# Performance work log

Hardware: AMD Instinct MI355X
Metric: run time of the kernel (lower is better)

## Reference

```python
import jax, jax.numpy as jnp
import numpy as np

BN_EPS = 1e-5
N_NODES = 100000
N_EDGES = 1600000
F_IN = 128
F_HID = 256
N_ITEMS = 128


def setup_inputs() -> dict:
    key = jax.random.key(0)
    ks = jax.random.split(key, 6)
    return {
        "node_feature": jax.random.normal(ks[0], (N_NODES, F_IN), jnp.float32),
        "edge_index": jax.random.randint(ks[1], (2, N_EDGES), 0, N_NODES, jnp.int64),
        "items_ready_to_cache": jnp.arange(N_ITEMS, dtype=jnp.int64),
        "gcn_w": jax.random.normal(ks[2], (F_IN, F_HID), jnp.float32) / np.sqrt(F_IN),
        "gcn_b": jnp.zeros((F_HID,), jnp.float32),
        "bn_gamma": jnp.ones((F_HID,), jnp.float32),
        "bn_beta": jnp.zeros((F_HID,), jnp.float32),
        "emb_table": jax.random.normal(ks[3], (F_IN, F_IN), jnp.float32),
        "proj_w": jax.random.normal(ks[4], (F_HID, F_IN), jnp.float32) / np.sqrt(F_HID),
        "proj_b": jnp.zeros((F_IN,), jnp.float32),
    }


def _gcn_conv(x, edge_index, w, b, n_nodes):
    # PyG GCNConv: add self-loops, symmetric normalization, scatter-add to target.
    loop = jnp.arange(n_nodes, dtype=edge_index.dtype)
    src = jnp.concatenate([edge_index[0], loop])
    dst = jnp.concatenate([edge_index[1], loop])
    h = x @ w                                  # [N, F_HID]
    deg = jax.ops.segment_sum(jnp.ones_like(dst, dtype=h.dtype), dst,
                              num_segments=n_nodes)
    dinv = jnp.where(deg > 0, jax.lax.rsqrt(deg), 0.0)
    norm = dinv[src] * dinv[dst]               # [E+N]
    msgs = h[src] * norm[:, None]              # gather + scale  [E+N, F_HID]
    out = jax.ops.segment_sum(msgs, dst, num_segments=n_nodes)  # scatter-add
    return out + b


def reference(node_feature, edge_index, items_ready_to_cache, gcn_w, gcn_b,
              bn_gamma, bn_beta, emb_table, proj_w, proj_b):
    n_nodes = node_feature.shape[0]
    x = _gcn_conv(node_feature, edge_index, gcn_w, gcn_b, n_nodes)
    # BatchNorm1d in training mode: batch stats (biased variance)
    mean = jnp.mean(x, axis=0)
    var = jnp.mean((x - mean) ** 2, axis=0)
    x = bn_gamma * (x - mean) * jax.lax.rsqrt(var + BN_EPS) + bn_beta
    x = jax.nn.relu(x)
    rsu_embedding = x[0:1] @ proj_w + proj_b   # [1, F_IN]
    # item_id_to_index collapses indices to arange(len(items))
    n_items = items_ready_to_cache.shape[0]
    items_embeddings = emb_table[jnp.arange(n_items)]  # [n_items, F_IN]
    scores = items_embeddings @ rsu_embedding[0]       # [n_items]
    return scores, rsu_embedding
```

## Files before the change

### kernel.cpp

```cpp
#include <hip/hip_runtime.h>
#include <hip/hip_bf16.h>


#define THREADS 256

__global__ __launch_bounds__(THREADS) void deg_kernel(const int* __restrict__ ei,
                                                      int* __restrict__ deg, int E, int N) {
    int e = blockIdx.x * THREADS + threadIdx.x;
    if (e < E) {
        unsigned d = (unsigned)ei[E + e];
        if (d < (unsigned)N) atomicAdd(&deg[d], 1);
    }
}

__global__ __launch_bounds__(THREADS) void dinv_kernel(const int* __restrict__ deg,
                                                       float* __restrict__ dinv, int n) {
    int i = blockIdx.x * THREADS + threadIdx.x;
    if (i < n) dinv[i] = rsqrtf((float)(deg[i] + 1));
}

__global__ __launch_bounds__(THREADS) void scan1_kernel(const int* __restrict__ deg,
                                                        int* __restrict__ rowptr,
                                                        int* __restrict__ bsum, int n) {
    __shared__ int sh[THREADS];
    const int t = threadIdx.x, b = blockIdx.x;
    const int base = b * 1024 + t * 4;
    int v0 = (base + 0 < n) ? deg[base + 0] : 0;
    int v1 = (base + 1 < n) ? deg[base + 1] : 0;
    int v2 = (base + 2 < n) ? deg[base + 2] : 0;
    int v3 = (base + 3 < n) ? deg[base + 3] : 0;
    const int local = v0 + v1 + v2 + v3;
    sh[t] = local;
    __syncthreads();
    int run = local;
    for (int off = 1; off < THREADS; off <<= 1) {
        int add = (t >= off) ? sh[t - off] : 0;
        __syncthreads();
        run += add;
        sh[t] = run;
        __syncthreads();
    }
    const int excl = run - local;
    if (base + 0 < n) rowptr[base + 0] = excl;
    if (base + 1 < n) rowptr[base + 1] = excl + v0;
    if (base + 2 < n) rowptr[base + 2] = excl + v0 + v1;
    if (base + 3 < n) rowptr[base + 3] = excl + v0 + v1 + v2;
    if (t == 0) bsum[b] = sh[THREADS - 1];
}

__global__ __launch_bounds__(THREADS) void scan2_kernel(const int* __restrict__ bsum,
                                                        int* __restrict__ boff, int nb) {
    __shared__ int sh[THREADS];
    const int t = threadIdx.x;
    const int local = (t < nb) ? bsum[t] : 0;
    sh[t] = local;
    __syncthreads();
    int run = local;
    for (int off = 1; off < THREADS; off <<= 1) {
        int add = (t >= off) ? sh[t - off] : 0;
        __syncthreads();
        run += add;
        sh[t] = run;
        __syncthreads();
    }
    boff[t] = run - local;
}

__global__ __launch_bounds__(THREADS) void scan3_kernel(int* __restrict__ rowptr,
                                                        int* __restrict__ cursor,
                                                        const int* __restrict__ boff,
                                                        int n, int E) {
    int i = blockIdx.x * THREADS + threadIdx.x;
    if (i < n) {
        int v = rowptr[i] + boff[i >> 10];
        rowptr[i] = v;
        cursor[i] = v;
    }
    if (i == 0) rowptr[n] = E;
}

__global__ __launch_bounds__(THREADS) void scatter_kernel(const int* __restrict__ ei,
                                                          int* __restrict__ cursor,
                                                          int* __restrict__ csr,
                                                          int E, int N) {
    int e = blockIdx.x * THREADS + threadIdx.x;
    if (e < E) {
        unsigned d = (unsigned)ei[E + e];
        if (d < (unsigned)N) {
            int p = atomicAdd(&cursor[d], 1);
            if ((unsigned)p < (unsigned)E) csr[p] = ei[e];
        }
    }
}

__device__ __forceinline__ float2 agg_row(const float* __restrict__ x,
                                          const int* __restrict__ rowptr,
                                          const int* __restrict__ csr,
                                          const float* __restrict__ dinv,
                                          int i, int n, int lane) {
    const int e0 = rowptr[i], e1 = rowptr[i + 1];
    const float di = dinv[i];
    const float2 xs = *(const float2*)(x + (size_t)i * 128 + lane * 2);
    float ax = di * xs.x, ay = di * xs.y;
    int e = e0;
    for (; e + 4 <= e1; e += 4) {
        int s0 = csr[e],     s1 = csr[e + 1], s2 = csr[e + 2], s3 = csr[e + 3];
        s0 = ((unsigned)s0 < (unsigned)n) ? s0 : 0;
        s1 = ((unsigned)s1 < (unsigned)n) ? s1 : 0;
        s2 = ((unsigned)s2 < (unsigned)n) ? s2 : 0;
        s3 = ((unsigned)s3 < (unsigned)n) ? s3 : 0;
        float w0 = dinv[s0], w1 = dinv[s1], w2 = dinv[s2], w3 = dinv[s3];
        float2 p0 = *(const float2*)(x + (size_t)s0 * 128 + lane * 2);
        float2 p1 = *(const float2*)(x + (size_t)s1 * 128 + lane * 2);
        float2 p2 = *(const float2*)(x + (size_t)s2 * 128 + lane * 2);
        float2 p3 = *(const float2*)(x + (size_t)s3 * 128 + lane * 2);
        ax = fmaf(w0, p0.x, ax); ay = fmaf(w0, p0.y, ay);
        ax = fmaf(w1, p1.x, ax); ay = fmaf(w1, p1.y, ay);
        ax = fmaf(w2, p2.x, ax); ay = fmaf(w2, p2.y, ay);
        ax = fmaf(w3, p3.x, ax); ay = fmaf(w3, p3.y, ay);
    }
    for (; e < e1; ++e) {
        int s = csr[e];
        s = ((unsigned)s < (unsigned)n) ? s : 0;
        float w = dinv[s];
        float2 p = *(const float2*)(x + (size_t)s * 128 + lane * 2);
        ax = fmaf(w, p.x, ax); ay = fmaf(w, p.y, ay);
    }
    return make_float2(di * ax, di * ay);
}

__global__ __launch_bounds__(THREADS) void agg_kernel(const float* __restrict__ x,
                                                      const int* __restrict__ rowptr,
                                                      const int* __restrict__ csr,
                                                      const float* __restrict__ dinv,
                                                      float* __restrict__ agg, int n) {
    const int lane = threadIdx.x & 63;
    const int wid  = blockIdx.x * (THREADS >> 6) + (threadIdx.x >> 6);
    const int nw   = gridDim.x * (THREADS >> 6);
    for (int i = wid; i < n; i += nw) {
        float2 o = agg_row(x, rowptr, csr, dinv, i, n, lane);
        *(float2*)(agg + (size_t)i * 128 + lane * 2) = o;
    }
}

__device__ __forceinline__ void gemm_epilogue(float acc[4][16], float* red,
                                              const float* __restrict__ bias,
                                              float* __restrict__ colsum,
                                              float* __restrict__ colsumsq,
                                              float* __restrict__ row0,
                                              int rowbase, int n, int tx, int ty, int t,
                                              int blockIdx_x) {
    bool valid[4];
#pragma unroll
    for (int i = 0; i < 4; ++i) valid[i] = (rowbase + ty * 4 + i) < n;
#pragma unroll
    for (int j = 0; j < 16; ++j) {
        float bj = bias[tx * 16 + j];
#pragma unroll
        for (int i = 0; i < 4; ++i)
            if (valid[i]) acc[i][j] += bj;
    }
    if (blockIdx_x == 0 && ty == 0) {
#pragma unroll
        for (int j = 0; j < 16; ++j) row0[tx * 16 + j] = acc[0][j];
    }
    float s[16], q[16];
#pragma unroll
    for (int j = 0; j < 16; ++j) {
        s[j] = 0.f; q[j] = 0.f;
#pragma unroll
        for (int i = 0; i < 4; ++i) {
            s[j] += acc[i][j];
            q[j] = fmaf(acc[i][j], acc[i][j], q[j]);
        }
    }
    float* redS = red;
    float* redQ = red + 16 * 256;
#pragma unroll
    for (int j = 0; j < 16; ++j) {
        redS[ty * 256 + tx * 16 + j] = s[j];
        redQ[ty * 256 + tx * 16 + j] = q[j];
    }
    __syncthreads();
    float S = 0.f, Q = 0.f;
#pragma unroll
    for (int g = 0; g < 16; ++g) {
        S += redS[g * 256 + t];
        Q += redQ[g * 256 + t];
    }
    atomicAdd(&colsum[t], S);
    atomicAdd(&colsumsq[t], Q);
}

__global__ __launch_bounds__(THREADS) void gemm_stats_kernel(
        const float* __restrict__ A, const float* __restrict__ W,
        const float* __restrict__ bias, float* __restrict__ colsum,
        float* __restrict__ colsumsq, float* __restrict__ row0, int n) {
    __shared__ float Asm[64 * 36];
    __shared__ float Bsm[32 * 320];
    const int t = threadIdx.x;
    const int tx = t & 15, ty = t >> 4;
    const int rowbase = blockIdx.x * 64;

    float acc[4][16];
#pragma unroll
    for (int i = 0; i < 4; ++i)
#pragma unroll
        for (int j = 0; j < 16; ++j) acc[i][j] = 0.0f;

    for (int kk = 0; kk < 128; kk += 32) {
#pragma unroll
        for (int u = 0; u < 2; ++u) {
            int f4 = t * 2 + u;
            int r = f4 >> 3, c4 = f4 & 7;
            int gr = rowbase + r;
            float4 v = make_float4(0.f, 0.f, 0.f, 0.f);
            if (gr < n) v = *(const float4*)(A + (size_t)gr * 128 + kk + c4 * 4);
            *(float4*)(Asm + r * 36 + c4 * 4) = v;
        }
#pragma unroll
        for (int u = 0; u < 8; ++u) {
            int f4 = t + u * 256;
            int k = f4 >> 6, c4 = f4 & 63;
            float4 v = *(const float4*)(W + (size_t)(kk + k) * 256 + c4 * 4);
            int blk = c4 >> 2, l = (c4 & 3) * 4;
            *(float4*)(Bsm + k * 320 + blk * 20 + l) = v;
        }
        __syncthreads();
#pragma unroll 4
        for (int k = 0; k < 32; ++k) {
            float a[4];
#pragma unroll
            for (int i = 0; i < 4; ++i) a[i] = Asm[(ty * 4 + i) * 36 + k];
            const float* bp = Bsm + k * 320 + tx * 20;
            float4 b0 = *(const float4*)(bp);
            float4 b1 = *(const float4*)(bp + 4);
            float4 b2 = *(const float4*)(bp + 8);
            float4 b3 = *(const float4*)(bp + 12);
            float bb[16] = {b0.x, b0.y, b0.z, b0.w, b1.x, b1.y, b1.z, b1.w,
                            b2.x, b2.y, b2.z, b2.w, b3.x, b3.y, b3.z, b3.w};
#pragma unroll
            for (int i = 0; i < 4; ++i)
#pragma unroll
                for (int j = 0; j < 16; ++j) acc[i][j] = fmaf(a[i], bb[j], acc[i][j]);
        }
        __syncthreads();
    }
    gemm_epilogue(acc, Bsm, bias, colsum, colsumsq, row0, rowbase, n, tx, ty, t,
                  blockIdx.x);
}

__global__ __launch_bounds__(THREADS) void fused_agg_gemm_kernel(
        const float* __restrict__ x, const int* __restrict__ rowptr,
        const int* __restrict__ csr, const float* __restrict__ dinv,
        const float* __restrict__ W, const float* __restrict__ bias,
        float* __restrict__ colsum, float* __restrict__ colsumsq,
        float* __restrict__ row0, int n) {
    __shared__ float Asm[64 * 132];
    __shared__ float Bsm[16 * 320];
    const int t = threadIdx.x;
    const int lane = t & 63, wv = t >> 6;
    const int tx = t & 15, ty = t >> 4;
    const int rowbase = blockIdx.x * 64;

    for (int rr = 0; rr < 16; ++rr) {
        const int r = wv * 16 + rr;
        const int i = rowbase + r;
        float2 o = make_float2(0.f, 0.f);
        if (i < n) o = agg_row(x, rowptr, csr, dinv, i, n, lane);
        *(float2*)(Asm + r * 132 + lane * 2) = o;
    }
    __syncthreads();

    float acc[4][16];
#pragma unroll
    for (int i = 0; i < 4; ++i)
#pragma unroll
        for (int j = 0; j < 16; ++j) acc[i][j] = 0.0f;

    for (int kk = 0; kk < 128; kk += 16) {
#pragma unroll
        for (int u = 0; u < 4; ++u) {
            int f4 = t + u * 256;
            int k = f4 >> 6, c4 = f4 & 63;
            float4 v = *(const float4*)(W + (size_t)(kk + k) * 256 + c4 * 4);
            int blk = c4 >> 2, l = (c4 & 3) * 4;
            *(float4*)(Bsm + k * 320 + blk * 20 + l) = v;
        }
        __syncthreads();
#pragma unroll 4
        for (int k = 0; k < 16; ++k) {
            float a[4];
#pragma unroll
            for (int i = 0; i < 4; ++i) a[i] = Asm[(ty * 4 + i) * 132 + kk + k];
            const float* bp = Bsm + k * 320 + tx * 20;
            float4 b0 = *(const float4*)(bp);
            float4 b1 = *(const float4*)(bp + 4);
            float4 b2 = *(const float4*)(bp + 8);
            float4 b3 = *(const float4*)(bp + 12);
            float bb[16] = {b0.x, b0.y, b0.z, b0.w, b1.x, b1.y, b1.z, b1.w,
                            b2.x, b2.y, b2.z, b2.w, b3.x, b3.y, b3.z, b3.w};
#pragma unroll
            for (int i = 0; i < 4; ++i)
#pragma unroll
                for (int j = 0; j < 16; ++j) acc[i][j] = fmaf(a[i], bb[j], acc[i][j]);
        }
        __syncthreads();
    }
    gemm_epilogue(acc, Asm, bias, colsum, colsumsq, row0, rowbase, n, tx, ty, t,
                  blockIdx.x);
}

__global__ __launch_bounds__(THREADS) void finalize_kernel(
        const float* __restrict__ colsum, const float* __restrict__ colsumsq,
        const float* __restrict__ row0, const float* __restrict__ gamma,
        const float* __restrict__ beta, const float* __restrict__ proj_w,
        const float* __restrict__ proj_b, const float* __restrict__ emb,
        float* __restrict__ out, int n_nodes, int n_items) {
    __shared__ float x0[256];
    __shared__ float rsu[128];
    const int t = threadIdx.x;
    const float invn = 1.0f / (float)n_nodes;
    {
        float mean = colsum[t] * invn;
        float var = colsumsq[t] * invn - mean * mean;
        float r = rsqrtf(var + 1e-5f);
        float v = gamma[t] * (row0[t] - mean) * r + beta[t];
        x0[t] = v > 0.f ? v : 0.f;
    }
    __syncthreads();
    if (t < 128) {
        float sacc = proj_b[t];
        for (int c = 0; c < 256; ++c) sacc = fmaf(x0[c], proj_w[c * 128 + t], sacc);
        rsu[t] = sacc;
        out[128 + t] = sacc;
    }
    __syncthreads();
    if (t < n_items) {
        float sacc = 0.f;
        for (int j = 0; j < 128; ++j) sacc = fmaf(emb[t * 128 + j], rsu[j], sacc);
        out[t] = sacc;
    }
}

extern "C" void kernel_launch(void* const* d_in, const int* in_sizes, int n_in,
                              void* d_out, int out_size, void* d_ws, size_t ws_size,
                              hipStream_t stream) {
    const float* node_feature = (const float*)d_in[0];
    const int*   edge_index   = (const int*)d_in[1];
    const float* gcn_w  = (const float*)d_in[3];
    const float* gcn_b  = (const float*)d_in[4];
    const float* bn_g   = (const float*)d_in[5];
    const float* bn_b   = (const float*)d_in[6];
    const float* emb    = (const float*)d_in[7];
    const float* proj_w = (const float*)d_in[8];
    const float* proj_b = (const float*)d_in[9];
    float* out = (float*)d_out;

    const int N = in_sizes[0] / 128;
    const int E = in_sizes[1] / 2;
    const int n_items = in_sizes[2];

    char* base = (char*)d_ws;
    size_t off = 0;
    auto alloc = [&](size_t bytes) -> void* {
        void* p = (void*)(base + off);
        off += (bytes + 255) & ~(size_t)255;
        return p;
    };
    int*   deg      = (int*)alloc((size_t)N * 4);
    float* dinv     = (float*)alloc((size_t)N * 4);
    int*   rowptr   = (int*)alloc(((size_t)N + 1) * 4);
    int*   cursor   = (int*)alloc((size_t)N * 4);
    int*   bsum     = (int*)alloc(256 * 4);
    int*   boff     = (int*)alloc(256 * 4);
    float* colsum   = (float*)alloc(256 * 4);
    float* colsumsq = (float*)alloc(256 * 4);
    float* row0     = (float*)alloc(256 * 4);
    int*   csr      = (int*)alloc((size_t)E * 4);
    const size_t fused_need = off;
    float* agg      = (float*)alloc((size_t)N * 128 * 4);
    const size_t split_need = off;
    const bool use_split = (ws_size >= split_need);
    (void)fused_need;

    const int nbE = (E + THREADS - 1) / THREADS;
    const int nbN = (N + THREADS - 1) / THREADS;
    const int nchunks = (N + 1023) >> 10;
    const int nbRow = (N + 63) / 64;

    hipMemsetAsync(deg, 0, (size_t)N * 4, stream);
    hipMemsetAsync(colsum, 0, 2 * 256 * 4, stream);

    deg_kernel<<<nbE, THREADS, 0, stream>>>(edge_index, deg, E, N);
    dinv_kernel<<<nbN, THREADS, 0, stream>>>(deg, dinv, N);
    scan1_kernel<<<nchunks, THREADS, 0, stream>>>(deg, rowptr, bsum, N);
    scan2_kernel<<<1, THREADS, 0, stream>>>(bsum, boff, nchunks);
    scan3_kernel<<<nbN, THREADS, 0, stream>>>(rowptr, cursor, boff, N, E);
    scatter_kernel<<<nbE, THREADS, 0, stream>>>(edge_index, cursor, csr, E, N);
    if (use_split) {
        agg_kernel<<<2048, THREADS, 0, stream>>>(node_feature, rowptr, csr, dinv,
                                                 agg, N);
        gemm_stats_kernel<<<nbRow, THREADS, 0, stream>>>(agg, gcn_w, gcn_b,
                                                         colsum, colsumsq, row0, N);
    } else {
        fused_agg_gemm_kernel<<<nbRow, THREADS, 0, stream>>>(node_feature, rowptr,
                                                             csr, dinv, gcn_w, gcn_b,
                                                             colsum, colsumsq, row0, N);
    }
    finalize_kernel<<<1, THREADS, 0, stream>>>(colsum, colsumsq, row0, bn_g, bn_b,
                                               proj_w, proj_b, emb, out, N, n_items);
}
```

Baseline: 522.1 us.

## Replace per-node GEMM with Gram-matrix statistics and rank-based CSR build

Instead of computing the full N x 256 GCN output, the aggregated features (128-wide) are reduced to a 128x128 Gram matrix and a column sum. BatchNorm mean and variance are then derived algebraically via W^T G W, with the bias term added analytically, and row 0 is computed separately. The CSR build records each edge's atomic rank during the degree pass, which removes the cursor atomics and the scan3 pass, and it folds dinv into scan1. The aggregation uses a persistent work-stealing kernel with per-block partial Grams that are reduced afterwards. The trade-off is some precision risk from the E[x^2]-mean^2 form and large partial-Gram workspace traffic.

```diff
diff --git a/kernel.cpp b/kernel.cpp
--- a/kernel.cpp
+++ b/kernel.cpp
@@ -4,24 +4,23 @@
 
 #define THREADS 256
 
-__global__ __launch_bounds__(THREADS) void deg_kernel(const int* __restrict__ ei,
-                                                      int* __restrict__ deg, int E, int N) {
+__global__ __launch_bounds__(THREADS) void deg_rank_kernel(const int* __restrict__ ei,
+                                                           int* __restrict__ deg,
+                                                           int* __restrict__ rank,
+                                                           int E, int N) {
     int e = blockIdx.x * THREADS + threadIdx.x;
     if (e < E) {
         unsigned d = (unsigned)ei[E + e];
-        if (d < (unsigned)N) atomicAdd(&deg[d], 1);
-    }
-}
-
-__global__ __launch_bounds__(THREADS) void dinv_kernel(const int* __restrict__ deg,
-                                                       float* __restrict__ dinv, int n) {
-    int i = blockIdx.x * THREADS + threadIdx.x;
-    if (i < n) dinv[i] = rsqrtf((float)(deg[i] + 1));
+        int p = 0;
+        if (d < (unsigned)N) p = atomicAdd(&deg[d], 1);
+        rank[e] = p;
+    }
 }
 
 __global__ __launch_bounds__(THREADS) void scan1_kernel(const int* __restrict__ deg,
                                                         int* __restrict__ rowptr,
-                                                        int* __restrict__ bsum, int n) {
+                                                        int* __restrict__ bsum,
+                                                        float* __restrict__ dinv, int n) {
     __shared__ int sh[THREADS];
     const int t = threadIdx.x, b = blockIdx.x;
     const int base = b * 1024 + t * 4;
@@ -29,6 +28,10 @@
     int v1 = (base + 1 < n) ? deg[base + 1] : 0;
     int v2 = (base + 2 < n) ? deg[base + 2] : 0;
     int v3 = (base + 3 < n) ? deg[base + 3] : 0;
+    if (base + 0 < n) dinv[base + 0] = rsqrtf((float)(v0 + 1));
+    if (base + 1 < n) dinv[base + 1] = rsqrtf((float)(v1 + 1));
+    if (base + 2 < n) dinv[base + 2] = rsqrtf((float)(v2 + 1));
+    if (base + 3 < n) dinv[base + 3] = rsqrtf((float)(v3 + 1));
     const int local = v0 + v1 + v2 + v3;
     sh[t] = local;
     __syncthreads();
@@ -49,7 +52,10 @@
 }
 
 __global__ __launch_bounds__(THREADS) void scan2_kernel(const int* __restrict__ bsum,
-                                                        int* __restrict__ boff, int nb) {
+                                                        int* __restrict__ boff, int nb,
+                                                        float* __restrict__ colsumS,
+                                                        float* __restrict__ G,
+                                                        int* __restrict__ workctr) {
     __shared__ int sh[THREADS];
     const int t = threadIdx.x;
     const int local = (t < nb) ? bsum[t] : 0;
@@ -64,251 +70,177 @@
         __syncthreads();
     }
     boff[t] = run - local;
-}
-
-__global__ __launch_bounds__(THREADS) void scan3_kernel(int* __restrict__ rowptr,
-                                                        int* __restrict__ cursor,
-                                                        const int* __restrict__ boff,
-                                                        int n, int E) {
-    int i = blockIdx.x * THREADS + threadIdx.x;
-    if (i < n) {
-        int v = rowptr[i] + boff[i >> 10];
-        rowptr[i] = v;
-        cursor[i] = v;
-    }
-    if (i == 0) rowptr[n] = E;
+    if (t < 128) colsumS[t] = 0.f;
+    if (t == 0) *workctr = 0;
+    for (int u = t; u < 16384; u += THREADS) G[u] = 0.f;
 }
 
 __global__ __launch_bounds__(THREADS) void scatter_kernel(const int* __restrict__ ei,
-                                                          int* __restrict__ cursor,
+                                                          const int* __restrict__ rowptr,
+                                                          const int* __restrict__ boff,
+                                                          const int* __restrict__ rank,
                                                           int* __restrict__ csr,
                                                           int E, int N) {
     int e = blockIdx.x * THREADS + threadIdx.x;
     if (e < E) {
         unsigned d = (unsigned)ei[E + e];
         if (d < (unsigned)N) {
-            int p = atomicAdd(&cursor[d], 1);
-            if ((unsigned)p < (unsigned)E) csr[p] = ei[e];
+            int base = rowptr[d] + boff[d >> 10] + rank[e];
+            if ((unsigned)base < (unsigned)E) csr[base] = ei[e];
         }
     }
 }
 
-__device__ __forceinline__ float2 agg_row(const float* __restrict__ x,
-                                          const int* __restrict__ rowptr,
-                                          const int* __restrict__ csr,
-                                          const float* __restrict__ dinv,
-                                          int i, int n, int lane) {
-    const int e0 = rowptr[i], e1 = rowptr[i + 1];
-    const float di = dinv[i];
-    const float2 xs = *(const float2*)(x + (size_t)i * 128 + lane * 2);
-    float ax = di * xs.x, ay = di * xs.y;
-    int e = e0;
-    for (; e + 4 <= e1; e += 4) {
-        int s0 = csr[e],     s1 = csr[e + 1], s2 = csr[e + 2], s3 = csr[e + 3];
-        s0 = ((unsigned)s0 < (unsigned)n) ? s0 : 0;
-        s1 = ((unsigned)s1 < (unsigned)n) ? s1 : 0;
-        s2 = ((unsigned)s2 < (unsigned)n) ? s2 : 0;
-        s3 = ((unsigned)s3 < (unsigned)n) ? s3 : 0;
-        float w0 = dinv[s0], w1 = dinv[s1], w2 = dinv[s2], w3 = dinv[s3];
-        float2 p0 = *(const float2*)(x + (size_t)s0 * 128 + lane * 2);
-        float2 p1 = *(const float2*)(x + (size_t)s1 * 128 + lane * 2);
-        float2 p2 = *(const float2*)(x + (size_t)s2 * 128 + lane * 2);
-        float2 p3 = *(const float2*)(x + (size_t)s3 * 128 + lane * 2);
-        ax = fmaf(w0, p0.x, ax); ay = fmaf(w0, p0.y, ay);
-        ax = fmaf(w1, p1.x, ax); ay = fmaf(w1, p1.y, ay);
-        ax = fmaf(w2, p2.x, ax); ay = fmaf(w2, p2.y, ay);
-        ax = fmaf(w3, p3.x, ax); ay = fmaf(w3, p3.y, ay);
-    }
-    for (; e < e1; ++e) {
-        int s = csr[e];
-        s = ((unsigned)s < (unsigned)n) ? s : 0;
-        float w = dinv[s];
-        float2 p = *(const float2*)(x + (size_t)s * 128 + lane * 2);
-        ax = fmaf(w, p.x, ax); ay = fmaf(w, p.y, ay);
-    }
-    return make_float2(di * ax, di * ay);
-}
-
-__global__ __launch_bounds__(THREADS) void agg_kernel(const float* __restrict__ x,
-                                                      const int* __restrict__ rowptr,
-                                                      const int* __restrict__ csr,
-                                                      const float* __restrict__ dinv,
-                                                      float* __restrict__ agg, int n) {
-    const int lane = threadIdx.x & 63;
-    const int wid  = blockIdx.x * (THREADS >> 6) + (threadIdx.x >> 6);
-    const int nw   = gridDim.x * (THREADS >> 6);
-    for (int i = wid; i < n; i += nw) {
-        float2 o = agg_row(x, rowptr, csr, dinv, i, n, lane);
-        *(float2*)(agg + (size_t)i * 128 + lane * 2) = o;
-    }
-}
-
-__device__ __forceinline__ void gemm_epilogue(float acc[4][16], float* red,
-                                              const float* __restrict__ bias,
-                                              float* __restrict__ colsum,
-                                              float* __restrict__ colsumsq,
-                                              float* __restrict__ row0,
-                                              int rowbase, int n, int tx, int ty, int t,
-                                              int blockIdx_x) {
-    bool valid[4];
-#pragma unroll
-    for (int i = 0; i < 4; ++i) valid[i] = (rowbase + ty * 4 + i) < n;
-#pragma unroll
-    for (int j = 0; j < 16; ++j) {
-        float bj = bias[tx * 16 + j];
-#pragma unroll
-        for (int i = 0; i < 4; ++i)
-            if (valid[i]) acc[i][j] += bj;
-    }
-    if (blockIdx_x == 0 && ty == 0) {
-#pragma unroll
-        for (int j = 0; j < 16; ++j) row0[tx * 16 + j] = acc[0][j];
-    }
-    float s[16], q[16];
-#pragma unroll
-    for (int j = 0; j < 16; ++j) {
-        s[j] = 0.f; q[j] = 0.f;
-#pragma unroll
-        for (int i = 0; i < 4; ++i) {
-            s[j] += acc[i][j];
-            q[j] = fmaf(acc[i][j], acc[i][j], q[j]);
-        }
-    }
-    float* redS = red;
-    float* redQ = red + 16 * 256;
-#pragma unroll
-    for (int j = 0; j < 16; ++j) {
-        redS[ty * 256 + tx * 16 + j] = s[j];
-        redQ[ty * 256 + tx * 16 + j] = q[j];
-    }
-    __syncthreads();
-    float S = 0.f, Q = 0.f;
-#pragma unroll
-    for (int g = 0; g < 16; ++g) {
-        S += redS[g * 256 + t];
-        Q += redQ[g * 256 + t];
-    }
-    atomicAdd(&colsum[t], S);
-    atomicAdd(&colsumsq[t], Q);
-}
-
-__global__ __launch_bounds__(THREADS) void gemm_stats_kernel(
-        const float* __restrict__ A, const float* __restrict__ W,
-        const float* __restrict__ bias, float* __restrict__ colsum,
-        float* __restrict__ colsumsq, float* __restrict__ row0, int n) {
-    __shared__ float Asm[64 * 36];
-    __shared__ float Bsm[32 * 320];
-    const int t = threadIdx.x;
-    const int tx = t & 15, ty = t >> 4;
-    const int rowbase = blockIdx.x * 64;
-
-    float acc[4][16];
-#pragma unroll
-    for (int i = 0; i < 4; ++i)
-#pragma unroll
-        for (int j = 0; j < 16; ++j) acc[i][j] = 0.0f;
-
-    for (int kk = 0; kk < 128; kk += 32) {
-#pragma unroll
-        for (int u = 0; u < 2; ++u) {
-            int f4 = t * 2 + u;
-            int r = f4 >> 3, c4 = f4 & 7;
-            int gr = rowbase + r;
-            float4 v = make_float4(0.f, 0.f, 0.f, 0.f);
-            if (gr < n) v = *(const float4*)(A + (size_t)gr * 128 + kk + c4 * 4);
-            *(float4*)(Asm + r * 36 + c4 * 4) = v;
-        }
-#pragma unroll
-        for (int u = 0; u < 8; ++u) {
-            int f4 = t + u * 256;
-            int k = f4 >> 6, c4 = f4 & 63;
-            float4 v = *(const float4*)(W + (size_t)(kk + k) * 256 + c4 * 4);
-            int blk = c4 >> 2, l = (c4 & 3) * 4;
-            *(float4*)(Bsm + k * 320 + blk * 20 + l) = v;
-        }
-        __syncthreads();
-#pragma unroll 4
-        for (int k = 0; k < 32; ++k) {
-            float a[4];
-#pragma unroll
-            for (int i = 0; i < 4; ++i) a[i] = Asm[(ty * 4 + i) * 36 + k];
-            const float* bp = Bsm + k * 320 + tx * 20;
-            float4 b0 = *(const float4*)(bp);
-            float4 b1 = *(const float4*)(bp + 4);
-            float4 b2 = *(const float4*)(bp + 8);
-            float4 b3 = *(const float4*)(bp + 12);
-            float bb[16] = {b0.x, b0.y, b0.z, b0.w, b1.x, b1.y, b1.z, b1.w,
-                            b2.x, b2.y, b2.z, b2.w, b3.x, b3.y, b3.z, b3.w};
-#pragma unroll
-            for (int i = 0; i < 4; ++i)
-#pragma unroll
-                for (int j = 0; j < 16; ++j) acc[i][j] = fmaf(a[i], bb[j], acc[i][j]);
-        }
-        __syncthreads();
-    }
-    gemm_epilogue(acc, Bsm, bias, colsum, colsumsq, row0, rowbase, n, tx, ty, t,
-                  blockIdx.x);
-}
-
-__global__ __launch_bounds__(THREADS) void fused_agg_gemm_kernel(
+__global__ __launch_bounds__(512) void agg_syrk_kernel(
         const float* __restrict__ x, const int* __restrict__ rowptr,
-        const int* __restrict__ csr, const float* __restrict__ dinv,
-        const float* __restrict__ W, const float* __restrict__ bias,
-        float* __restrict__ colsum, float* __restrict__ colsumsq,
-        float* __restrict__ row0, int n) {
+        const int* __restrict__ boff, const int* __restrict__ csr,
+        const float* __restrict__ dinv, int* __restrict__ workctr,
+        float* __restrict__ Gpart, float* __restrict__ colsumS,
+        float* __restrict__ agg0, int n, int E, int NC) {
     __shared__ float Asm[64 * 132];
-    __shared__ float Bsm[16 * 320];
+    __shared__ int sh_c;
     const int t = threadIdx.x;
     const int lane = t & 63, wv = t >> 6;
-    const int tx = t & 15, ty = t >> 4;
-    const int rowbase = blockIdx.x * 64;
-
-    for (int rr = 0; rr < 16; ++rr) {
-        const int r = wv * 16 + rr;
-        const int i = rowbase + r;
-        float2 o = make_float2(0.f, 0.f);
-        if (i < n) o = agg_row(x, rowptr, csr, dinv, i, n, lane);
-        *(float2*)(Asm + r * 132 + lane * 2) = o;
-    }
-    __syncthreads();
-
-    float acc[4][16];
-#pragma unroll
-    for (int i = 0; i < 4; ++i)
-#pragma unroll
-        for (int j = 0; j < 16; ++j) acc[i][j] = 0.0f;
-
-    for (int kk = 0; kk < 128; kk += 16) {
-#pragma unroll
-        for (int u = 0; u < 4; ++u) {
-            int f4 = t + u * 256;
-            int k = f4 >> 6, c4 = f4 & 63;
-            float4 v = *(const float4*)(W + (size_t)(kk + k) * 256 + c4 * 4);
-            int blk = c4 >> 2, l = (c4 & 3) * 4;
-            *(float4*)(Bsm + k * 320 + blk * 20 + l) = v;
+    const int p0 = (t >> 5) * 8;
+    const int q0 = (t & 31) * 4;
+    const float* xl = x + lane * 2;
+
+    float acc[8][4];
+#pragma unroll
+    for (int i = 0; i < 8; ++i)
+#pragma unroll
+        for (int j = 0; j < 4; ++j) acc[i][j] = 0.f;
+    float s_acc = 0.f;
+
+    for (;;) {
+        if (t == 0) sh_c = atomicAdd(workctr, 1);
+        __syncthreads();
+        const int c = sh_c;
+        if (c >= NC) break;
+
+        for (int rr = 0; rr < 8; ++rr) {
+            const int r = wv * 8 + rr;
+            const int i = c * 64 + r;
+            float ax = 0.f, ay = 0.f;
+            if (i < n) {
+                const int e0 = rowptr[i] + boff[i >> 10];
+                const int e1 = (i + 1 < n) ? rowptr[i + 1] + boff[(i + 1) >> 10] : E;
+                const float di = dinv[i];
+                const float2 xs = *(const float2*)(xl + (size_t)i * 128);
+                ax = di * xs.x; ay = di * xs.y;
+                int e = e0;
+                for (; e + 8 <= e1; e += 8) {
+                    int ss[8]; float ww[8]; float2 pv[8];
+#pragma unroll
+                    for (int u = 0; u < 8; ++u) {
+                        int s = csr[e + u];
+                        ss[u] = ((unsigned)s < (unsigned)n) ? s : 0;
+                    }
+#pragma unroll
+                    for (int u = 0; u < 8; ++u) ww[u] = dinv[ss[u]];
+#pragma unroll
+                    for (int u = 0; u < 8; ++u)
+                        pv[u] = *(const float2*)(xl + (size_t)ss[u] * 128);
+#pragma unroll
+                    for (int u = 0; u < 8; ++u) {
+                        ax = fmaf(ww[u], pv[u].x, ax);
+                        ay = fmaf(ww[u], pv[u].y, ay);
+                    }
+                }
+                for (; e < e1; ++e) {
+                    int s = csr[e];
+                    s = ((unsigned)s < (unsigned)n) ? s : 0;
+                    float w = dinv[s];
+                    float2 p = *(const float2*)(xl + (size_t)s * 128);
+                    ax = fmaf(w, p.x, ax);
+                    ay = fmaf(w, p.y, ay);
+                }
+                ax *= di; ay *= di;
+            }
+            *(float2*)(Asm + r * 132 + lane * 2) = make_float2(ax, ay);
         }
         __syncthreads();
+
+        if (c == 0 && t < 32)
+            *(float4*)(agg0 + t * 4) = *(const float4*)(Asm + t * 4);
+
 #pragma unroll 4
-        for (int k = 0; k < 16; ++k) {
-            float a[4];
-#pragma unroll
-            for (int i = 0; i < 4; ++i) a[i] = Asm[(ty * 4 + i) * 132 + kk + k];
-            const float* bp = Bsm + k * 320 + tx * 20;
-            float4 b0 = *(const float4*)(bp);
-            float4 b1 = *(const float4*)(bp + 4);
-            float4 b2 = *(const float4*)(bp + 8);
-            float4 b3 = *(const float4*)(bp + 12);
-            float bb[16] = {b0.x, b0.y, b0.z, b0.w, b1.x, b1.y, b1.z, b1.w,
-                            b2.x, b2.y, b2.z, b2.w, b3.x, b3.y, b3.z, b3.w};
-#pragma unroll
-            for (int i = 0; i < 4; ++i)
-#pragma unroll
-                for (int j = 0; j < 16; ++j) acc[i][j] = fmaf(a[i], bb[j], acc[i][j]);
+        for (int r = 0; r < 64; ++r) {
+            const float* row = Asm + r * 132;
+            float4 a0 = *(const float4*)(row + p0);
+            float4 a1 = *(const float4*)(row + p0 + 4);
+            float4 bq = *(const float4*)(row + q0);
+            float ap[8] = {a0.x, a0.y, a0.z, a0.w, a1.x, a1.y, a1.z, a1.w};
+            float aq[4] = {bq.x, bq.y, bq.z, bq.w};
+#pragma unroll
+            for (int pp = 0; pp < 8; ++pp)
+#pragma unroll
+                for (int qq = 0; qq < 4; ++qq)
+                    acc[pp][qq] = fmaf(ap[pp], aq[qq], acc[pp][qq]);
         }
-        __syncthreads();
-    }
-    gemm_epilogue(acc, Asm, bias, colsum, colsumsq, row0, rowbase, n, tx, ty, t,
-                  blockIdx.x);
+        if (t < 128) {
+            float sa = 0.f;
+            for (int r = 0; r < 64; ++r) sa += Asm[r * 132 + t];
+            s_acc += sa;
+        }
+        __syncthreads();
+    }
+
+    float* gp = Gpart + (size_t)blockIdx.x * 16384;
+#pragma unroll
+    for (int pp = 0; pp < 8; ++pp)
+        *(float4*)(gp + (p0 + pp) * 128 + q0) =
+            make_float4(acc[pp][0], acc[pp][1], acc[pp][2], acc[pp][3]);
+    if (t < 128) atomicAdd(&colsumS[t], s_acc);
+}
+
+__global__ __launch_bounds__(THREADS) void greduce_kernel(const float* __restrict__ Gpart,
+                                                          float* __restrict__ G, int NB) {
+    const int seg = blockIdx.x >> 4;
+    const int i4 = (blockIdx.x & 15) * THREADS + threadIdx.x;
+    const int b0 = (seg * NB) / 8, b1 = ((seg + 1) * NB) / 8;
+    float4 a = make_float4(0.f, 0.f, 0.f, 0.f);
+    for (int b = b0; b < b1; ++b) {
+        float4 v = *(const float4*)(Gpart + (size_t)b * 16384 + i4 * 4);
+        a.x += v.x; a.y += v.y; a.z += v.z; a.w += v.w;
+    }
+    atomicAdd(&G[i4 * 4 + 0], a.x);
+    atomicAdd(&G[i4 * 4 + 1], a.y);
+    atomicAdd(&G[i4 * 4 + 2], a.z);
+    atomicAdd(&G[i4 * 4 + 3], a.w);
+}
+
+__global__ __launch_bounds__(THREADS) void stats_kernel(
+        const float* __restrict__ G, const float* __restrict__ W,
+        const float* __restrict__ bias, const float* __restrict__ colsumS,
+        const float* __restrict__ agg0, float* __restrict__ colsum,
+        float* __restrict__ colsumsq, float* __restrict__ row0, int n) {
+    __shared__ float wsm[128];
+    __shared__ float red[THREADS], red2[THREADS], red3[THREADS];
+    const int t = threadIdx.x, j = blockIdx.x;
+    if (t < 128) wsm[t] = W[t * 256 + j];
+    __syncthreads();
+    float part = 0.f;
+    const float wq = wsm[t & 127];
+    const int pbase = t >> 7;
+#pragma unroll 8
+    for (int u = 0; u < 64; ++u)
+        part = fmaf(G[u * 256 + t], wsm[pbase + u * 2], part);
+    red[t] = part * wq;
+    red2[t] = (t < 128) ? colsumS[t] * wsm[t] : 0.f;
+    red3[t] = (t < 128) ? agg0[t] * wsm[t] : 0.f;
+    __syncthreads();
+    for (int s = 128; s > 0; s >>= 1) {
+        if (t < s) { red[t] += red[t + s]; red2[t] += red2[t + s]; red3[t] += red3[t + s]; }
+        __syncthreads();
+    }
+    if (t == 0) {
+        const float b = bias[j];
+        const float sw = red2[0];
+        colsum[j]   = sw + (float)n * b;
+        colsumsq[j] = red[0] + 2.f * b * sw + (float)n * b * b;
+        row0[j]     = red3[0] + b;
+    }
 }
 
 __global__ __launch_bounds__(THREADS) void finalize_kernel(
@@ -369,45 +301,39 @@
         return p;
     };
     int*   deg      = (int*)alloc((size_t)N * 4);
-    float* dinv     = (float*)alloc((size_t)N * 4);
-    int*   rowptr   = (int*)alloc(((size_t)N + 1) * 4);
-    int*   cursor   = (int*)alloc((size_t)N * 4);
+    int*   rank     = (int*)alloc((size_t)E * 4);
+    int*   rowptr   = (int*)alloc((size_t)N * 4);
     int*   bsum     = (int*)alloc(256 * 4);
     int*   boff     = (int*)alloc(256 * 4);
+    float* dinv     = (float*)alloc((size_t)N * 4);
+    int*   csr      = (int*)alloc((size_t)E * 4);
+    float* colsumS  = (float*)alloc(128 * 4);
+    float* agg0     = (float*)alloc(128 * 4);
+    float* G        = (float*)alloc(16384 * 4);
     float* colsum   = (float*)alloc(256 * 4);
     float* colsumsq = (float*)alloc(256 * 4);
     float* row0     = (float*)alloc(256 * 4);
-    int*   csr      = (int*)alloc((size_t)E * 4);
-    const size_t fused_need = off;
-    float* agg      = (float*)alloc((size_t)N * 128 * 4);
-    const size_t split_need = off;
-    const bool use_split = (ws_size >= split_need);
-    (void)fused_need;
+    int*   workctr  = (int*)alloc(256);
+    int NB = (int)((ws_size > off) ? ((ws_size - off) / (16384 * 4)) : 0);
+    if (NB > 512) NB = 512;
+    if (NB < 8) NB = 8;
+    float* Gpart    = (float*)alloc((size_t)NB * 16384 * 4);
 
     const int nbE = (E + THREADS - 1) / THREADS;
-    const int nbN = (N + THREADS - 1) / THREADS;
     const int nchunks = (N + 1023) >> 10;
-    const int nbRow = (N + 63) / 64;
+    const int NC = (N + 63) / 64;
 
     hipMemsetAsync(deg, 0, (size_t)N * 4, stream);
-    hipMemsetAsync(colsum, 0, 2 * 256 * 4, stream);
-
-    deg_kernel<<<nbE, THREADS, 0, stream>>>(edge_index, deg, E, N);
-    dinv_kernel<<<nbN, THREADS, 0, stream>>>(deg, dinv, N);
-    scan1_kernel<<<nchunks, THREADS, 0, stream>>>(deg, rowptr, bsum, N);
-    scan2_kernel<<<1, THREADS, 0, stream>>>(bsum, boff, nchunks);
-    scan3_kernel<<<nbN, THREADS, 0, stream>>>(rowptr, cursor, boff, N, E);
-    scatter_kernel<<<nbE, THREADS, 0, stream>>>(edge_index, cursor, csr, E, N);
-    if (use_split) {
-        agg_kernel<<<2048, THREADS, 0, stream>>>(node_feature, rowptr, csr, dinv,
-                                                 agg, N);
-        gemm_stats_kernel<<<nbRow, THREADS, 0, stream>>>(agg, gcn_w, gcn_b,
-                                                         colsum, colsumsq, row0, N);
-    } else {
-        fused_agg_gemm_kernel<<<nbRow, THREADS, 0, stream>>>(node_feature, rowptr,
-                                                             csr, dinv, gcn_w, gcn_b,
-                                                             colsum, colsumsq, row0, N);
-    }
+
+    deg_rank_kernel<<<nbE, THREADS, 0, stream>>>(edge_index, deg, rank, E, N);
+    scan1_kernel<<<nchunks, THREADS, 0, stream>>>(deg, rowptr, bsum, dinv, N);
+    scan2_kernel<<<1, THREADS, 0, stream>>>(bsum, boff, nchunks, colsumS, G, workctr);
+    scatter_kernel<<<nbE, THREADS, 0, stream>>>(edge_index, rowptr, boff, rank, csr, E, N);
+    agg_syrk_kernel<<<NB, 512, 0, stream>>>(node_feature, rowptr, boff, csr, dinv,
+                                            workctr, Gpart, colsumS, agg0, N, E, NC);
+    greduce_kernel<<<128, THREADS, 0, stream>>>(Gpart, G, NB);
+    stats_kernel<<<256, THREADS, 0, stream>>>(G, gcn_w, gcn_b, colsumS, agg0,
+                                              colsum, colsumsq, row0, N);
     finalize_kernel<<<1, THREADS, 0, stream>>>(colsum, colsumsq, row0, bn_g, bn_b,
                                                proj_w, proj_b, emb, out, N, n_items);
 }
```

New measurement: 421.7 us. 1.24x faster.
